# Performance work log

Measured on AMD Instinct MI355X. Metric: run time of the kernel, lower is better.

The kernel has to match this reference:

```python
import jax, jax.numpy as jnp
import numpy as np

EPS = 1e-5

def _bn(x, g, b, m, v):
    # inference-mode batchnorm with moving statistics
    return (x - m) * jax.lax.rsqrt(v + EPS) * g + b

def setup_inputs() -> dict:
    key = jax.random.key(0)
    ks = jax.random.split(key, 12)
    t, b, s, hu = 512, 64, 1024, 1024
    d_in = s + hu
    si = jax.random.normal(ks[0], (b, s), dtype=jnp.float32)
    h = jax.random.normal(ks[1], (t, b, hu), dtype=jnp.float32)
    W0 = jax.random.normal(ks[2], (d_in, 10), dtype=jnp.float32) * 0.02
    b0 = jnp.zeros((10,), jnp.float32)
    g0 = jnp.ones((10,), jnp.float32)
    be0 = jnp.zeros((10,), jnp.float32)
    m0 = jax.random.normal(ks[3], (10,), dtype=jnp.float32) * 0.1
    v0 = jax.random.uniform(ks[4], (10,), dtype=jnp.float32) + 0.5
    W1 = jax.random.normal(ks[5], (10, 5), dtype=jnp.float32) * 0.3
    b1 = jnp.zeros((5,), jnp.float32)
    g1 = jnp.ones((5,), jnp.float32)
    be1 = jnp.zeros((5,), jnp.float32)
    m1 = jax.random.normal(ks[6], (5,), dtype=jnp.float32) * 0.1
    v1 = jax.random.uniform(ks[7], (5,), dtype=jnp.float32) + 0.5
    W2 = jax.random.normal(ks[8], (5, 1), dtype=jnp.float32) * 0.4
    b2 = jnp.zeros((1,), jnp.float32)
    return {"si": si, "h": h, "W0": W0, "b0": b0, "g0": g0, "be0": be0,
            "m0": m0, "v0": v0, "W1": W1, "b1": b1, "g1": g1, "be1": be1,
            "m1": m1, "v1": v1, "W2": W2, "b2": b2}

def reference(si, h, W0, b0, g0, be0, m0, v0, W1, b1, g1, be1, m1, v1, W2, b2):
    t, b, hu = h.shape
    # concat decoder state with every encoder hidden state: [t, b, s+hu]
    x = jnp.concatenate([jnp.broadcast_to(si[None], (t,) + si.shape), h], axis=-1)
    x = jax.nn.relu(_bn(x @ W0 + b0, g0, be0, m0, v0))
    x = jax.nn.relu(_bn(x @ W1 + b1, g1, be1, m1, v1))
    scores = x @ W2 + b2                       # [t, b, 1]
    # original: tf.concat over axis 0 -> [t*b, 1], softmax over axis 0 (ALL t*b entries)
    a = jax.nn.softmax(scores.reshape(t * b))  # [t*b]
    # original uses only the first t rows of the flattened softmax as scalar weights
    ci = jnp.einsum('t,tbh->bh', a[:t], h)     # [b, hu]
    return ci
```

## Files before the change

kernel.cpp:

```cpp
#include <hip/hip_runtime.h>

#define EPS 1e-5f

constexpr int T  = 512;
constexpr int B  = 64;
constexpr int HU = 1024;
constexpr int S  = 1024;
constexpr int C  = B * HU;
constexpr int TCHUNK = 64;
constexpr int NTC = T / TCHUNK;
constexpr int KC  = 128;
constexpr int NCH = HU / KC;
constexpr int LDR = KC + 1;

constexpr size_t OFF_SIW0 = 0;
constexpr size_t OFF_W    = 1024;
constexpr size_t OFF_ESC  = 2048;
constexpr size_t OFF_PART = 35840;

__device__ __forceinline__ float mlp_head(
    const float* __restrict__ u10,
    const float* __restrict__ b0, const float* __restrict__ g0,
    const float* __restrict__ be0,const float* __restrict__ m0,
    const float* __restrict__ v0,
    const float* __restrict__ W1, const float* __restrict__ b1,
    const float* __restrict__ g1, const float* __restrict__ be1,
    const float* __restrict__ m1, const float* __restrict__ v1,
    const float* __restrict__ W2, const float* __restrict__ b2) {
    float y[10];
#pragma unroll
    for (int j = 0; j < 10; ++j) {
        float u = (u10[j] + b0[j] - m0[j]) * (1.0f / sqrtf(v0[j] + EPS)) * g0[j]
                  + be0[j];
        y[j] = fmaxf(u, 0.f);
    }
    float z[5];
#pragma unroll
    for (int i = 0; i < 5; ++i) {
        float u = b1[i];
#pragma unroll
        for (int j = 0; j < 10; ++j) u = fmaf(y[j], W1[j * 5 + i], u);
        u = (u - m1[i]) * (1.0f / sqrtf(v1[i] + EPS)) * g1[i] + be1[i];
        z[i] = fmaxf(u, 0.f);
    }
    float sc = b2[0];
#pragma unroll
    for (int i = 0; i < 5; ++i) sc = fmaf(z[i], W2[i], sc);
    return sc;
}

__global__ __launch_bounds__(256) void k_weights(
    const float* __restrict__ h,  const float* __restrict__ si,
    const float* __restrict__ W0,
    const float* __restrict__ b0, const float* __restrict__ g0,
    const float* __restrict__ be0,const float* __restrict__ m0,
    const float* __restrict__ v0,
    const float* __restrict__ W1, const float* __restrict__ b1,
    const float* __restrict__ g1, const float* __restrict__ be1,
    const float* __restrict__ m1, const float* __restrict__ v1,
    const float* __restrict__ W2, const float* __restrict__ b2,
    float* __restrict__ w, float* __restrict__ siW0out) {
    const int e   = blockIdx.x;
    const int t   = e >> 6;
    const int cb  = e & 63;
    const int tid = threadIdx.x;
    const int wv  = tid >> 6, ln = tid & 63;

    const float4 hv = *(const float4*)(h  + (size_t)t  * C + (size_t)cb * HU + tid * 4);
    const float4 sv = *(const float4*)(si + (size_t)cb * S + tid * 4);
    const float* wsb = W0 + (size_t)(4 * tid) * 10;
    const float* whb = W0 + (size_t)(1024 + 4 * tid) * 10;

    float ssi[10], shh[10];
#pragma unroll
    for (int j = 0; j < 10; ++j) { ssi[j] = 0.f; shh[j] = 0.f; }
#pragma unroll
    for (int d = 0; d < 4; ++d) {
        const float sx = (&sv.x)[d], hx = (&hv.x)[d];
#pragma unroll
        for (int j = 0; j < 10; ++j) {
            ssi[j] = fmaf(sx, wsb[d * 10 + j], ssi[j]);
            shh[j] = fmaf(hx, whb[d * 10 + j], shh[j]);
        }
    }
#pragma unroll
    for (int j = 0; j < 10; ++j) {
#pragma unroll
        for (int off = 32; off > 0; off >>= 1) {
            ssi[j] += __shfl_down(ssi[j], off, 64);
            shh[j] += __shfl_down(shh[j], off, 64);
        }
    }
    __shared__ float rs[4][10], rh[4][10];
    if (ln == 0) {
#pragma unroll
        for (int j = 0; j < 10; ++j) { rs[wv][j] = ssi[j]; rh[wv][j] = shh[j]; }
    }
    __syncthreads();

    if (t == 0 && tid < 10)
        siW0out[cb * 10 + tid] = rs[0][tid] + rs[1][tid] + rs[2][tid] + rs[3][tid];

    if (tid == 0) {
        float u10[10];
#pragma unroll
        for (int j = 0; j < 10; ++j)
            u10[j] = rs[0][j] + rs[1][j] + rs[2][j] + rs[3][j] +
                     rh[0][j] + rh[1][j] + rh[2][j] + rh[3][j];
        const float sc = mlp_head(u10, b0, g0, be0, m0, v0,
                                  W1, b1, g1, be1, m1, v1, W2, b2);
        w[t * 64 + cb] = expf(sc);
    }
}

__global__ __launch_bounds__(512) void k_mega(
    const float* __restrict__ h,  const float* __restrict__ W0,
    const float* __restrict__ w,  const float* __restrict__ siW0,
    const float* __restrict__ b0, const float* __restrict__ g0,
    const float* __restrict__ be0,const float* __restrict__ m0,
    const float* __restrict__ v0,
    const float* __restrict__ W1, const float* __restrict__ b1,
    const float* __restrict__ g1, const float* __restrict__ be1,
    const float* __restrict__ m1, const float* __restrict__ v1,
    const float* __restrict__ W2, const float* __restrict__ b2,
    float* __restrict__ escore, float* __restrict__ part) {
    const int b   = blockIdx.x & 63;
    const int tc  = blockIdx.x >> 6;
    const int tid = threadIdx.x;
    const int wv  = tid >> 6;
    const int ln  = tid & 63;

    __shared__ float sh[64 * LDR];
    __shared__ float park[8][64][10];
    __shared__ float wsl[64];

    if (tid < 64) wsl[tid] = w[tc * 64 + tid];

    const float* hb = h + (size_t)(tc * 64) * C + (size_t)b * HU;
    const int srow  = tid >> 5;
    const int slane = tid & 31;

    float stg[16];
#pragma unroll
    for (int q = 0; q < 4; ++q)
#pragma unroll
        for (int d = 0; d < 4; ++d)
            stg[4 * q + d] = hb[(size_t)(16 * q + srow) * C + 32 * d + slane];

    const int klo = __builtin_amdgcn_readfirstlane(16 * wv);
    const int kk  = tid >> 2;
    const int qtr = tid & 3;

    float sacc[10];
#pragma unroll
    for (int j = 0; j < 10; ++j) sacc[j] = 0.f;

    for (int c = 0; c < NCH; ++c) {
        if (c > 0) __syncthreads();
#pragma unroll
        for (int q = 0; q < 4; ++q)
#pragma unroll
            for (int d = 0; d < 4; ++d)
                sh[(16 * q + srow) * LDR + 32 * d + slane] = stg[4 * q + d];
        if (c + 1 < NCH) {
#pragma unroll
            for (int q = 0; q < 4; ++q)
#pragma unroll
                for (int d = 0; d < 4; ++d)
                    stg[4 * q + d] = hb[(size_t)(16 * q + srow) * C +
                                        (c + 1) * KC + 32 * d + slane];
        }
        __syncthreads();

        const float* wp  = W0 + (size_t)(1024 + c * KC + klo) * 10;
        const float* shp = sh + ln * LDR + klo;
#pragma unroll
        for (int i = 0; i < 16; ++i) {
            const float hx = shp[i];
#pragma unroll
            for (int j = 0; j < 10; ++j)
                sacc[j] = fmaf(hx, wp[i * 10 + j], sacc[j]);
        }

        float s = 0.f;
        const float* shc = sh + (16 * qtr) * LDR + kk;
        const float* wl  = wsl + 16 * qtr;
#pragma unroll
        for (int r = 0; r < 16; ++r)
            s = fmaf(wl[r], shc[r * LDR], s);
        s += __shfl_xor(s, 1, 64);
        s += __shfl_xor(s, 2, 64);
        if (qtr == 0)
            part[(size_t)tc * C + (size_t)b * HU + c * KC + kk] = s;
    }

#pragma unroll
    for (int j = 0; j < 10; ++j) park[wv][ln][j] = sacc[j];
    __syncthreads();
    if (tid < 64) {
        float u10[10];
#pragma unroll
        for (int j = 0; j < 10; ++j)
            u10[j] = park[0][tid][j] + park[1][tid][j] + park[2][tid][j] +
                     park[3][tid][j] + park[4][tid][j] + park[5][tid][j] +
                     park[6][tid][j] + park[7][tid][j] + siW0[b * 10 + j];
        const float sc = mlp_head(u10, b0, g0, be0, m0, v0,
                                  W1, b1, g1, be1, m1, v1, W2, b2);
        escore[(size_t)(tc * 64 + tid) * 64 + b] = expf(sc);
    }
}

__global__ __launch_bounds__(256) void k_out(const float* __restrict__ part,
                                             const float* __restrict__ escore,
                                             float* __restrict__ out) {
    const int tid = threadIdx.x;
    const int wv  = tid >> 6, ln = tid & 63;

    float zs = 0.f;
#pragma unroll
    for (int q = 0; q < 32; ++q) {
        const float4 v = ((const float4*)escore)[tid + 256 * q];
        zs += v.x + v.y + v.z + v.w;
    }
#pragma unroll
    for (int off = 32; off > 0; off >>= 1)
        zs += __shfl_down(zs, off, 64);
    __shared__ float zr[4];
    __shared__ float sinv;
    if (ln == 0) zr[wv] = zs;
    __syncthreads();
    if (tid == 0) sinv = 1.0f / (zr[0] + zr[1] + zr[2] + zr[3]);
    __syncthreads();
    const float invZ = sinv;

    const int c = blockIdx.x * 1024 + tid * 4;
    float4 s = {0.f, 0.f, 0.f, 0.f};
#pragma unroll
    for (int ts = 0; ts < NTC; ++ts) {
        const float4 v = *(const float4*)(part + (size_t)ts * C + c);
        s.x += v.x; s.y += v.y; s.z += v.z; s.w += v.w;
    }
    s.x *= invZ; s.y *= invZ; s.z *= invZ; s.w *= invZ;
    *(float4*)(out + c) = s;
}

extern "C" void kernel_launch(void* const* d_in, const int* in_sizes, int n_in,
                              void* d_out, int out_size, void* d_ws, size_t ws_size,
                              hipStream_t stream) {
    const float* si  = (const float*)d_in[0];
    const float* h   = (const float*)d_in[1];
    const float* W0  = (const float*)d_in[2];
    const float* b0  = (const float*)d_in[3];
    const float* g0  = (const float*)d_in[4];
    const float* be0 = (const float*)d_in[5];
    const float* m0  = (const float*)d_in[6];
    const float* v0  = (const float*)d_in[7];
    const float* W1  = (const float*)d_in[8];
    const float* b1  = (const float*)d_in[9];
    const float* g1  = (const float*)d_in[10];
    const float* be1 = (const float*)d_in[11];
    const float* m1  = (const float*)d_in[12];
    const float* v1  = (const float*)d_in[13];
    const float* W2  = (const float*)d_in[14];
    const float* b2  = (const float*)d_in[15];

    float* ws     = (float*)d_ws;
    float* siW0   = ws + OFF_SIW0;
    float* w      = ws + OFF_W;
    float* escore = ws + OFF_ESC;
    float* part   = ws + OFF_PART;
    float* out    = (float*)d_out;

    hipLaunchKernelGGL(k_weights, dim3(512), dim3(256), 0, stream, h, si, W0,
                       b0, g0, be0, m0, v0, W1, b1, g1, be1, m1, v1, W2, b2,
                       w, siW0);
    hipLaunchKernelGGL(k_mega,    dim3(512), dim3(512), 0, stream, h, W0, w, siW0,
                       b0, g0, be0, m0, v0, W1, b1, g1, be1, m1, v1, W2, b2,
                       escore, part);
    hipLaunchKernelGGL(k_out,     dim3(64),  dim3(256), 0, stream, part, escore, out);
}
```

Measured before the change: 250.4 us.

## Halve K-chunk and alias shared buffers to raise k_mega occupancy

Reduces the per-iteration K chunk from 128 to 64 columns, halving the register staging array and the shared tile. The tile and the per-wave partial-sum area now share one aliased shared buffer, and launch bounds request more resident blocks per CU. The aim is more waves in flight to hide global-load latency. In exchange it doubles the number of chunk iterations and barriers, adds an extra shuffle stage, and issues smaller loads per iteration.

```diff
diff --git a/kernel.cpp b/kernel.cpp
--- a/kernel.cpp
+++ b/kernel.cpp
@@ -9,7 +9,7 @@
 constexpr int C  = B * HU;
 constexpr int TCHUNK = 64;
 constexpr int NTC = T / TCHUNK;
-constexpr int KC  = 128;
+constexpr int KC  = 64;
 constexpr int NCH = HU / KC;
 constexpr int LDR = KC + 1;
 
@@ -113,7 +113,7 @@
     }
 }
 
-__global__ __launch_bounds__(512) void k_mega(
+__global__ __launch_bounds__(512, 8) void k_mega(
     const float* __restrict__ h,  const float* __restrict__ W0,
     const float* __restrict__ w,  const float* __restrict__ siW0,
     const float* __restrict__ b0, const float* __restrict__ g0,
@@ -130,8 +130,7 @@
     const int wv  = tid >> 6;
     const int ln  = tid & 63;
 
-    __shared__ float sh[64 * LDR];
-    __shared__ float park[8][64][10];
+    __shared__ float buf[5248];
     __shared__ float wsl[64];
 
     if (tid < 64) wsl[tid] = w[tc * 64 + tid];
@@ -140,16 +139,16 @@
     const int srow  = tid >> 5;
     const int slane = tid & 31;
 
-    float stg[16];
+    float stg[8];
 #pragma unroll
     for (int q = 0; q < 4; ++q)
 #pragma unroll
-        for (int d = 0; d < 4; ++d)
-            stg[4 * q + d] = hb[(size_t)(16 * q + srow) * C + 32 * d + slane];
-
-    const int klo = __builtin_amdgcn_readfirstlane(16 * wv);
-    const int kk  = tid >> 2;
-    const int qtr = tid & 3;
+        for (int d = 0; d < 2; ++d)
+            stg[2 * q + d] = hb[(size_t)(16 * q + srow) * C + 32 * d + slane];
+
+    const int klo = __builtin_amdgcn_readfirstlane(8 * wv);
+    const int kk  = tid >> 3;
+    const int oct = tid & 7;
 
     float sacc[10];
 #pragma unroll
@@ -160,22 +159,22 @@
 #pragma unroll
         for (int q = 0; q < 4; ++q)
 #pragma unroll
-            for (int d = 0; d < 4; ++d)
-                sh[(16 * q + srow) * LDR + 32 * d + slane] = stg[4 * q + d];
+            for (int d = 0; d < 2; ++d)
+                buf[(16 * q + srow) * LDR + 32 * d + slane] = stg[2 * q + d];
         if (c + 1 < NCH) {
 #pragma unroll
             for (int q = 0; q < 4; ++q)
 #pragma unroll
-                for (int d = 0; d < 4; ++d)
-                    stg[4 * q + d] = hb[(size_t)(16 * q + srow) * C +
+                for (int d = 0; d < 2; ++d)
+                    stg[2 * q + d] = hb[(size_t)(16 * q + srow) * C +
                                         (c + 1) * KC + 32 * d + slane];
         }
         __syncthreads();
 
         const float* wp  = W0 + (size_t)(1024 + c * KC + klo) * 10;
-        const float* shp = sh + ln * LDR + klo;
-#pragma unroll
-        for (int i = 0; i < 16; ++i) {
+        const float* shp = buf + ln * LDR + klo;
+#pragma unroll
+        for (int i = 0; i < 8; ++i) {
             const float hx = shp[i];
 #pragma unroll
             for (int j = 0; j < 10; ++j)
@@ -183,27 +182,31 @@
         }
 
         float s = 0.f;
-        const float* shc = sh + (16 * qtr) * LDR + kk;
-        const float* wl  = wsl + 16 * qtr;
-#pragma unroll
-        for (int r = 0; r < 16; ++r)
+        const float* shc = buf + (8 * oct) * LDR + kk;
+        const float* wl  = wsl + 8 * oct;
+#pragma unroll
+        for (int r = 0; r < 8; ++r)
             s = fmaf(wl[r], shc[r * LDR], s);
         s += __shfl_xor(s, 1, 64);
         s += __shfl_xor(s, 2, 64);
-        if (qtr == 0)
+        s += __shfl_xor(s, 4, 64);
+        if (oct == 0)
             part[(size_t)tc * C + (size_t)b * HU + c * KC + kk] = s;
     }
 
-#pragma unroll
-    for (int j = 0; j < 10; ++j) park[wv][ln][j] = sacc[j];
+    __syncthreads();
+#pragma unroll
+    for (int j = 0; j < 10; ++j) buf[(wv * 64 + ln) * 10 + j] = sacc[j];
     __syncthreads();
     if (tid < 64) {
         float u10[10];
 #pragma unroll
-        for (int j = 0; j < 10; ++j)
-            u10[j] = park[0][tid][j] + park[1][tid][j] + park[2][tid][j] +
-                     park[3][tid][j] + park[4][tid][j] + park[5][tid][j] +
-                     park[6][tid][j] + park[7][tid][j] + siW0[b * 10 + j];
+        for (int j = 0; j < 10; ++j) {
+            float u = siW0[b * 10 + j];
+#pragma unroll
+            for (int wq = 0; wq < 8; ++wq) u += buf[(wq * 64 + tid) * 10 + j];
+            u10[j] = u;
+        }
         const float sc = mlp_head(u10, b0, g0, be0, m0, v0,
                                   W1, b1, g1, be1, m1, v1, W2, b2);
         escore[(size_t)(tc * 64 + tid) * 64 + b] = expf(sc);
```

After: 252.3 us. No clear change (+0.7%).
